# Kernel tuning notes

Hardware: AMD Instinct MI355X
Metric: run time of the kernel (lower is better)

The kernel has to match this reference:

```python
import jax, jax.numpy as jnp
import numpy as np

DIM_K = 32


def setup_inputs() -> dict:
    N, DORI, DAPP, DK, NCLS = 4096, 2048, 512, 32, 21
    key = jax.random.key(0)
    ks = jax.random.split(key, 16)
    std = 0.01
    inp = {
        'rois': jax.random.normal(ks[0], (N, 5), jnp.float32),
        'delta_rois': jax.random.normal(ks[1], (9, N, 5), jnp.float32),
        'features': jax.random.normal(ks[2], (9, N, DORI), jnp.float32),
        'gt_features': jax.random.normal(ks[3], (1, N, DORI), jnp.float32),
        'ious': jax.random.uniform(ks[4], (9, 1, N), jnp.float32),
        # learned parameters (singleton broadcast dims squeezed out)
        'attention_feat': jax.random.normal(ks[5], (DORI, DAPP), jnp.float32) * std,
        'w_k': jax.random.normal(ks[6], (DAPP, DK, 4), jnp.float32) * std,
        'w_q': jax.random.normal(ks[7], (9, DAPP, DK, 4), jnp.float32) * std,
        'alpha_w': jax.random.normal(ks[8], (9, DORI, 4), jnp.float32) * std,
        'bbox_regress': jax.random.normal(ks[9], (9, DORI, 4), jnp.float32) * 0.001,
        'w_k_cls': jax.random.normal(ks[10], (DAPP, DK, 1), jnp.float32) * std,
        'w_q_cls': jax.random.normal(ks[11], (9, DAPP, DK, 1), jnp.float32) * std,
        'alpha_w_cls': jax.random.normal(ks[12], (9, DORI, 1), jnp.float32) * std,
        'cls_score_w': jax.random.normal(ks[13], (9, DORI, NCLS), jnp.float32) * std,
    }
    return inp


def reference(rois, delta_rois, features, gt_features, ious,
              attention_feat, w_k, w_q, alpha_w, bbox_regress,
              w_k_cls, w_q_cls, alpha_w_cls, cls_score_w):
    # features: (9, N, DORI). The torch code materializes (9,N,DORI,DAPP)
    # via broadcast-mul + sum; einsum computes the identical contraction.
    off = jax.nn.relu(jnp.einsum('anf,fd->and', features, attention_feat))  # (9,N,DAPP)

    alpha = jnp.einsum('anf,afc->anc', features, alpha_w)          # (9,N,4)
    offset = jnp.einsum('anf,afc->anc', features, bbox_regress)   # (9,N,4)
    alpha_softmax = jax.nn.softmax(alpha, axis=0)
    delta8 = delta_rois[:, :, 1:5]                                  # (9,N,4)
    delta_pred_offset = delta8 + offset
    output = jnp.sum(delta_pred_offset * alpha_softmax, axis=0)    # (N,4)

    # ---- classification branch ----
    cls_score = jnp.einsum('anf,afc->anc', features, cls_score_w)  # (9,N,NCLS)
    alpha_cls = jnp.einsum('anf,afc->anc', features, alpha_w_cls)  # (9,N,1)
    alpha_softmax_cls = jax.nn.softmax(alpha_cls, axis=0)

    # ---- training-only beta (query/key) attention ----
    query_out = jnp.einsum('and,adkc->ankc', off, w_q)          # (9,N,DK,4)
    query_out_cls = jnp.einsum('and,adkc->ankc', off, w_q_cls)  # (9,N,DK,1)
    gt_off = jax.nn.relu(jnp.einsum('nf,fd->nd', gt_features[0], attention_feat))  # (N,DAPP)
    key_out = jnp.einsum('nd,dkc->nkc', gt_off, w_k)            # (N,DK,4)
    key_out_cls = jnp.einsum('nd,dkc->nkc', gt_off, w_k_cls)    # (N,DK,1)

    scale = 1.0 / np.sqrt(DIM_K).astype(np.float32)
    beta_out = jnp.einsum('ankc,nkc->anc', query_out, key_out) * scale - ious[:, 0, :, None]  # (9,N,4)
    beta_softmax = jax.nn.softmax(beta_out, axis=0)
    beta_out_cls = jnp.einsum('ankc,nkc->anc', query_out_cls, key_out_cls) * scale - ious.reshape(9, -1, 1)  # (9,N,1)
    beta_softmax_cls = jax.nn.softmax(beta_out_cls, axis=0)

    output_beta = jnp.sum(delta_pred_offset * beta_softmax, axis=0)  # (N,4)

    return (output, output_beta, alpha_softmax, beta_softmax,
            delta_pred_offset, delta_pred_offset, alpha, beta_out,
            cls_score, alpha_softmax_cls, beta_softmax_cls, alpha_cls, beta_out_cls)
```

## Files before the change

kernel.cpp:

```cpp
#include <hip/hip_runtime.h>

using u16 = unsigned short;
using s16x8 = __attribute__((ext_vector_type(8))) short;
using f32x4 = __attribute__((ext_vector_type(4))) float;

#define DEVI __device__ __forceinline__

constexpr int AN = 9, NB = 10, NN = 4096, DORI = 2048, DAPP = 512, NCLS = 21, QCOLS = 160;

constexpr size_t O0 = 0;
constexpr size_t O1 = 16384;
constexpr size_t O2 = 32768;
constexpr size_t O3 = 180224;
constexpr size_t O4 = 327680;
constexpr size_t O5 = 475136;
constexpr size_t O6 = 622592;
constexpr size_t O7 = 770048;
constexpr size_t O8 = 917504;
constexpr size_t O9 = 1691648;
constexpr size_t O10 = 1728512;
constexpr size_t O11 = 1765376;
constexpr size_t O12 = 1802240;

constexpr int CAST_B = 36864;
constexpr int ATT_B  = 256;
constexpr int PQ_B   = 3200;
constexpr int PS_B   = 72;
constexpr int GT_B   = 4096;
constexpr int PREP_TOTAL = CAST_B + ATT_B + PQ_B + PS_B + GT_B;

DEVI u16 f2b(float f) {
  unsigned u = __float_as_uint(f);
  unsigned r = (u + 0x7fffu + ((u >> 16) & 1u)) >> 16;
  return (u16)r;
}

DEVI uint4 pack8(float4 u, float4 v) {
  uint4 r;
  r.x = (unsigned)f2b(u.x) | ((unsigned)f2b(u.y) << 16);
  r.y = (unsigned)f2b(u.z) | ((unsigned)f2b(u.w) << 16);
  r.z = (unsigned)f2b(v.x) | ((unsigned)f2b(v.y) << 16);
  r.w = (unsigned)f2b(v.z) | ((unsigned)f2b(v.w) << 16);
  return r;
}

DEVI void gload_lds16(const u16* g, u16* l) {
  __builtin_amdgcn_global_load_lds(
      (const __attribute__((address_space(1))) void*)g,
      (__attribute__((address_space(3))) void*)l, 16, 0, 0);
}

__global__ __launch_bounds__(256) void prep_cast(const float* __restrict__ features,
                                                 const float* __restrict__ att,
                                                 const float* __restrict__ wq,
                                                 const float* __restrict__ wqc,
                                                 const float* __restrict__ wk,
                                                 const float* __restrict__ wkc,
                                                 const float* __restrict__ aw,
                                                 const float* __restrict__ bb,
                                                 const float* __restrict__ awc,
                                                 const float* __restrict__ cw,
                                                 const float* __restrict__ gt,
                                                 u16* __restrict__ featB,
                                                 u16* __restrict__ attB,
                                                 u16* __restrict__ Wq,
                                                 u16* __restrict__ Wsm) {
  __shared__ float tile[64][65];
  const int b = blockIdx.x, tid = threadIdx.x;
  if (b < CAST_B) {
    if (!featB) return;
    long i = (long)b * 256 + tid;
    float4 v0 = ((const float4*)features)[i * 2];
    float4 v1 = ((const float4*)features)[i * 2 + 1];
    ((uint4*)featB)[i] = pack8(v0, v1);
  } else if (b < CAST_B + ATT_B) {
    int b2 = b - CAST_B;
    int d0 = (b2 >> 3) * 64, c0 = (b2 & 7) * 64;
#pragma unroll
    for (int r = 0; r < 16; ++r) {
      int dl = r * 4 + (tid >> 6), cl = tid & 63;
      tile[dl][cl] = att[(size_t)(d0 + dl) * DAPP + c0 + cl];
    }
    __syncthreads();
#pragma unroll
    for (int w = 0; w < 16; ++w) {
      int cl = w * 4 + (tid >> 6), dl = tid & 63;
      attB[(size_t)(c0 + cl) * DORI + d0 + dl] = f2b(tile[dl][cl]);
    }
  } else if (b < CAST_B + ATT_B + PQ_B) {
    int t = (b - CAST_B - ATT_B) * 256 + tid;
    int bq = t / (QCOLS * DAPP);
    int r = t % (QCOLS * DAPP);
    int col = r / DAPP, d = r % DAPP;
    float v;
    if (bq < 9) {
      if (col < 128) v = wq[(size_t)bq * DAPP * 128 + (size_t)d * 128 + col];
      else           v = wqc[(size_t)bq * DAPP * 32 + (size_t)d * 32 + (col - 128)];
    } else {
      if (col < 128) v = wk[(size_t)d * 128 + col];
      else           v = wkc[(size_t)d * 32 + (col - 128)];
    }
    Wq[t] = f2b(v);
  } else if (b < CAST_B + ATT_B + PQ_B + PS_B) {
    int t = (b - CAST_B - ATT_B - PQ_B) * 256 + tid;
    if (t >= AN * DORI) return;
    int a = t / DORI, f = t % DORI;
    u16* Wa = Wsm + (size_t)a * 32 * DORI;
    for (int c = 0; c < 4; ++c)  Wa[c * DORI + f]       = f2b(aw[((size_t)a * DORI + f) * 4 + c]);
    for (int c = 0; c < 4; ++c)  Wa[(4 + c) * DORI + f] = f2b(bb[((size_t)a * DORI + f) * 4 + c]);
    for (int c = 0; c < 21; ++c) Wa[(8 + c) * DORI + f] = f2b(cw[((size_t)a * DORI + f) * 21 + c]);
    Wa[29 * DORI + f] = f2b(awc[(size_t)a * DORI + f]);
    Wa[30 * DORI + f] = 0;
    Wa[31 * DORI + f] = 0;
  } else {
    if (!featB) return;
    long i = (long)(b - CAST_B - ATT_B - PQ_B - PS_B) * 256 + tid;
    float4 v0 = ((const float4*)gt)[i * 2];
    float4 v1 = ((const float4*)gt)[i * 2 + 1];
    ((uint4*)(featB + (size_t)AN * NN * DORI))[i] = pack8(v0, v1);
  }
}

__global__ __launch_bounds__(256) void gemm_main(const u16* __restrict__ featB,
                                                 const u16* __restrict__ attB,
                                                 const u16* __restrict__ Wsm,
                                                 u16* __restrict__ offb,
                                                 float* __restrict__ smallf,
                                                 float* __restrict__ cls_out) {
  __shared__ __align__(16) u16 As[128 * 32];
  __shared__ __align__(16) u16 Bs[128 * 32];

  int bx = blockIdx.x, by = blockIdx.y, bz = blockIdx.z;
  {
    int h = bx + 5 * (by + 32 * bz);
    int l = (h & 7) * 200 + (h >> 3);
    bx = l % 5; l /= 5; by = l % 32; bz = l / 32;
  }
  const int tid = threadIdx.x, lane = tid & 63, w = tid >> 6;
  const bool small = (bx == 4);
  if (small && bz == 9) return;
  const int tileM = by * 128;
  const u16* Ab = featB + ((size_t)bz * NN + tileM) * DORI;
  const u16* Bb = small ? (Wsm + (size_t)bz * 32 * DORI)
                        : (attB + (size_t)bx * 128 * DORI);

  f32x4 accM[4][4], accS[2][2];
#pragma unroll
  for (int i = 0; i < 4; ++i)
#pragma unroll
    for (int j = 0; j < 4; ++j) accM[i][j] = (f32x4){0.f, 0.f, 0.f, 0.f};
#pragma unroll
  for (int i = 0; i < 2; ++i)
#pragma unroll
    for (int j = 0; j < 2; ++j) accS[i][j] = (f32x4){0.f, 0.f, 0.f, 0.f};

  const int wm = w & 1, wn = w >> 1;
  const u16* ArM = As + (wm * 64 + (lane & 15)) * 32 + (lane >> 4) * 8;
  const u16* BrM = Bs + (wn * 64 + (lane & 15)) * 32 + (lane >> 4) * 8;
  const u16* ArS = As + (w * 32 + (lane & 15)) * 32 + (lane >> 4) * 8;
  const u16* BrS = Bs + ((lane & 15)) * 32 + (lane >> 4) * 8;

  for (int k0 = 0; k0 < DORI; k0 += 32) {
#pragma unroll
    for (int i = 0; i < 2; ++i) {
      int c = tid + i * 256;
      gload_lds16(Ab + (size_t)(c >> 2) * DORI + k0 + (c & 3) * 8, As + c * 8);
    }
    if (small) {
      if (tid < 128)
        gload_lds16(Bb + (size_t)(tid >> 2) * DORI + k0 + (tid & 3) * 8, Bs + tid * 8);
    } else {
#pragma unroll
      for (int i = 0; i < 2; ++i) {
        int c = tid + i * 256;
        gload_lds16(Bb + (size_t)(c >> 2) * DORI + k0 + (c & 3) * 8, Bs + c * 8);
      }
    }
    __syncthreads();
    if (small) {
      s16x8 af[2], bf[2];
#pragma unroll
      for (int i = 0; i < 2; ++i) af[i] = *(const s16x8*)(ArS + i * 16 * 32);
#pragma unroll
      for (int j = 0; j < 2; ++j) bf[j] = *(const s16x8*)(BrS + j * 16 * 32);
#pragma unroll
      for (int i = 0; i < 2; ++i)
#pragma unroll
        for (int j = 0; j < 2; ++j)
          accS[i][j] = __builtin_amdgcn_mfma_f32_16x16x32_bf16(af[i], bf[j], accS[i][j], 0, 0, 0);
    } else {
      s16x8 af[4], bf[4];
#pragma unroll
      for (int i = 0; i < 4; ++i) af[i] = *(const s16x8*)(ArM + i * 16 * 32);
#pragma unroll
      for (int j = 0; j < 4; ++j) bf[j] = *(const s16x8*)(BrM + j * 16 * 32);
#pragma unroll
      for (int i = 0; i < 4; ++i)
#pragma unroll
        for (int j = 0; j < 4; ++j)
          accM[i][j] = __builtin_amdgcn_mfma_f32_16x16x32_bf16(af[i], bf[j], accM[i][j], 0, 0, 0);
    }
    __syncthreads();
  }

  if (small) {
#pragma unroll
    for (int i = 0; i < 2; ++i)
#pragma unroll
      for (int j = 0; j < 2; ++j)
#pragma unroll
        for (int q = 0; q < 4; ++q) {
          const int row = tileM + w * 32 + i * 16 + (lane >> 4) * 4 + q;
          const int col = j * 16 + (lane & 15);
          const size_t an = (size_t)bz * NN + row;
          float v = accS[i][j][q];
          smallf[an * 32 + col] = v;
          if (col >= 8 && col <= 28) cls_out[an * 21 + (col - 8)] = v;
        }
  } else {
    const int r0 = tileM + wm * 64 + (lane >> 4) * 4;
    const int c0 = bx * 128 + wn * 64 + (lane & 15);
#pragma unroll
    for (int i = 0; i < 4; ++i)
#pragma unroll
      for (int j = 0; j < 4; ++j)
#pragma unroll
        for (int q = 0; q < 4; ++q)
          offb[((size_t)bz * NN + r0 + i * 16 + q) * DAPP + c0 + j * 16] =
              f2b(fmaxf(accM[i][j][q], 0.f));
  }
}

template<int BM, int BN, int WM, int WN, bool RELU, bool OUTBF, bool SWZ>
__global__ __launch_bounds__(WM * WN * 64)
void gemm_glds(const u16* __restrict__ A, long sA, const u16* __restrict__ B, long sB,
               void* __restrict__ Cv, long sC, int N, int K) {
  constexpr int THREADS = WM * WN * 64;
  constexpr int WTM = BM / WM, WTN = BN / WN;
  constexpr int FM = WTM / 16, FN = WTN / 16;
  constexpr int ACHN = BM * 4, BCHN = BN * 4;
  constexpr int ACH = (ACHN + THREADS - 1) / THREADS;
  constexpr int BCH = (BCHN + THREADS - 1) / THREADS;
  constexpr bool AFULL = (ACHN % THREADS) == 0, BFULL = (BCHN % THREADS) == 0;

  __shared__ __align__(16) u16 As[BM * 32];
  __shared__ __align__(16) u16 Bs[BN * 32];

  int bx = blockIdx.x, by = blockIdx.y, bz = blockIdx.z;
  if constexpr (SWZ) {
    int gx = gridDim.x, gy = gridDim.y;
    int h = bx + gx * (by + gy * bz);
    int nwg = gx * gy * (int)gridDim.z;
    int cpx = nwg >> 3;
    int l = (h & 7) * cpx + (h >> 3);
    bx = l % gx; l /= gx; by = l % gy; bz = l / gy;
  }

  const int tid = threadIdx.x, lane = tid & 63, wave = tid >> 6;
  const int wm = wave % WM, wn = wave / WM;
  const int tileN = bx * BN, tileM = by * BM;
  const u16* Ab = A + (size_t)bz * sA + (size_t)tileM * K;
  const u16* Bb = B + (size_t)bz * sB + (size_t)tileN * K;

  f32x4 acc[FM][FN];
#pragma unroll
  for (int i = 0; i < FM; ++i)
#pragma unroll
    for (int j = 0; j < FN; ++j) acc[i][j] = (f32x4){0.f, 0.f, 0.f, 0.f};

  const u16* Arow = As + (wm * WTM + (lane & 15)) * 32 + (lane >> 4) * 8;
  const u16* Brow = Bs + (wn * WTN + (lane & 15)) * 32 + (lane >> 4) * 8;

  for (int k0 = 0; k0 < K; k0 += 32) {
#pragma unroll
    for (int i = 0; i < ACH; ++i) {
      int c = tid + i * THREADS;
      if (AFULL || c < ACHN)
        gload_lds16(Ab + (size_t)(c >> 2) * K + k0 + (c & 3) * 8, As + c * 8);
    }
#pragma unroll
    for (int i = 0; i < BCH; ++i) {
      int c = tid + i * THREADS;
      if (BFULL || c < BCHN)
        gload_lds16(Bb + (size_t)(c >> 2) * K + k0 + (c & 3) * 8, Bs + c * 8);
    }
    __syncthreads();
    s16x8 af[FM], bfr[FN];
#pragma unroll
    for (int i = 0; i < FM; ++i) af[i] = *(const s16x8*)(Arow + i * 16 * 32);
#pragma unroll
    for (int j = 0; j < FN; ++j) bfr[j] = *(const s16x8*)(Brow + j * 16 * 32);
#pragma unroll
    for (int i = 0; i < FM; ++i)
#pragma unroll
      for (int j = 0; j < FN; ++j)
        acc[i][j] = __builtin_amdgcn_mfma_f32_16x16x32_bf16(af[i], bfr[j], acc[i][j], 0, 0, 0);
    __syncthreads();
  }

  const int r0 = tileM + wm * WTM + (lane >> 4) * 4;
  const int c0 = tileN + wn * WTN + (lane & 15);
#pragma unroll
  for (int i = 0; i < FM; ++i)
#pragma unroll
    for (int j = 0; j < FN; ++j)
#pragma unroll
      for (int q = 0; q < 4; ++q) {
        float v = acc[i][j][q];
        if (RELU) v = fmaxf(v, 0.f);
        size_t idx = (size_t)bz * sC + (size_t)(r0 + i * 16 + q) * N + (c0 + j * 16);
        if (OUTBF) ((u16*)Cv)[idx] = f2b(v);
        else       ((float*)Cv)[idx] = v;
      }
}

template<int BM, int BN, int WM, int WN, bool RELU, bool OUTBF>
__global__ __launch_bounds__(WM * WN * 64)
void gemm_af32(const float* __restrict__ Av, const float* __restrict__ A2v, long sA,
               const u16* __restrict__ B, long sB,
               void* __restrict__ Cv, long sC, int N, int K) {
  constexpr int THREADS = WM * WN * 64;
  constexpr int WTM = BM / WM, WTN = BN / WN;
  constexpr int FM = WTM / 16, FN = WTN / 16;
  constexpr int ACH = (BM * 4) / THREADS;
  constexpr int BCHN = BN * 4;
  constexpr int BCH = (BCHN + THREADS - 1) / THREADS;
  constexpr bool BFULL = (BCHN % THREADS) == 0;

  __shared__ __align__(16) u16 As[BM * 32];
  __shared__ __align__(16) u16 Bs[BN * 32];

  const int tid = threadIdx.x, lane = tid & 63, wave = tid >> 6;
  const int wm = wave % WM, wn = wave / WM;
  const int tileN = blockIdx.x * BN, tileM = blockIdx.y * BM;
  const int batch = blockIdx.z;
  const float* base = (batch < 9) ? (Av + (size_t)batch * sA) : A2v;
  const float* Ab32 = base + (size_t)tileM * K;
  const u16* Bb = B + (size_t)batch * sB + (size_t)tileN * K;

  f32x4 acc[FM][FN];
#pragma unroll
  for (int i = 0; i < FM; ++i)
#pragma unroll
    for (int j = 0; j < FN; ++j) acc[i][j] = (f32x4){0.f, 0.f, 0.f, 0.f};

  uint4 ra[ACH], rb[BCH];
  auto load_t = [&](int k0) {
#pragma unroll
    for (int i = 0; i < ACH; ++i) {
      int c = tid + i * THREADS;
      const float* s = Ab32 + (size_t)(c >> 2) * K + k0 + (c & 3) * 8;
      ra[i] = pack8(*(const float4*)s, *(const float4*)(s + 4));
    }
#pragma unroll
    for (int i = 0; i < BCH; ++i) {
      int c = tid + i * THREADS;
      if (BFULL || c < BCHN)
        rb[i] = *(const uint4*)(Bb + (size_t)(c >> 2) * K + k0 + (c & 3) * 8);
    }
  };

  load_t(0);
  const u16* Arow = As + (wm * WTM + (lane & 15)) * 32 + (lane >> 4) * 8;
  const u16* Brow = Bs + (wn * WTN + (lane & 15)) * 32 + (lane >> 4) * 8;

  for (int k0 = 0; k0 < K; k0 += 32) {
    __syncthreads();
#pragma unroll
    for (int i = 0; i < ACH; ++i)
      *(uint4*)(As + (size_t)(tid + i * THREADS) * 8) = ra[i];
#pragma unroll
    for (int i = 0; i < BCH; ++i) {
      int c = tid + i * THREADS;
      if (BFULL || c < BCHN) *(uint4*)(Bs + (size_t)c * 8) = rb[i];
    }
    __syncthreads();
    if (k0 + 32 < K) load_t(k0 + 32);
    s16x8 af[FM], bfr[FN];
#pragma unroll
    for (int i = 0; i < FM; ++i) af[i] = *(const s16x8*)(Arow + i * 16 * 32);
#pragma unroll
    for (int j = 0; j < FN; ++j) bfr[j] = *(const s16x8*)(Brow + j * 16 * 32);
#pragma unroll
    for (int i = 0; i < FM; ++i)
#pragma unroll
      for (int j = 0; j < FN; ++j)
        acc[i][j] = __builtin_amdgcn_mfma_f32_16x16x32_bf16(af[i], bfr[j], acc[i][j], 0, 0, 0);
  }

  const int r0 = tileM + wm * WTM + (lane >> 4) * 4;
  const int c0 = tileN + wn * WTN + (lane & 15);
#pragma unroll
  for (int i = 0; i < FM; ++i)
#pragma unroll
    for (int j = 0; j < FN; ++j)
#pragma unroll
      for (int q = 0; q < 4; ++q) {
        float v = acc[i][j][q];
        if (RELU) v = fmaxf(v, 0.f);
        size_t idx = (size_t)batch * sC + (size_t)(r0 + i * 16 + q) * N + (c0 + j * 16);
        if (OUTBF) ((u16*)Cv)[idx] = f2b(v);
        else       ((float*)Cv)[idx] = v;
      }
}

__global__ __launch_bounds__(256) void cls_copy(const float* __restrict__ smallf,
                                                float* __restrict__ o) {
  int i = blockIdx.x * blockDim.x + threadIdx.x;
  if (i >= AN * NN * NCLS) return;
  int an = i / NCLS, c = i % NCLS;
  o[i] = smallf[(size_t)an * 32 + 8 + c];
}

__global__ __launch_bounds__(256) void gemm2qb(const u16* __restrict__ offb,
                                               const u16* __restrict__ Wq,
                                               const float* __restrict__ keyf,
                                               const float* __restrict__ ious,
                                               float* __restrict__ betaf,
                                               float* __restrict__ betac) {
  constexpr int BM = 128, BN = 160;
  __shared__ __align__(16) u16 As[BM * 32];
  __shared__ __align__(16) u16 Bs[BN * 32];
  const int tid = threadIdx.x, lane = tid & 63, wave = tid >> 6;
  const int tileM = blockIdx.x * BM;
  const int a = blockIdx.y;
  const u16* Ab = offb + ((size_t)a * NN + tileM) * DAPP;
  const u16* Bb = Wq + (size_t)a * QCOLS * DAPP;

  f32x4 acc[2][10];
#pragma unroll
  for (int i = 0; i < 2; ++i)
#pragma unroll
    for (int j = 0; j < 10; ++j) acc[i][j] = (f32x4){0.f, 0.f, 0.f, 0.f};

  const u16* Arow = As + (wave * 32 + (lane & 15)) * 32 + (lane >> 4) * 8;
  const u16* Brow = Bs + (lane & 15) * 32 + (lane >> 4) * 8;

  for (int k0 = 0; k0 < DAPP; k0 += 32) {
#pragma unroll
    for (int i = 0; i < 2; ++i) {
      int c = tid + i * 256;
      gload_lds16(Ab + (size_t)(c >> 2) * DAPP + k0 + (c & 3) * 8, As + c * 8);
    }
#pragma unroll
    for (int i = 0; i < 3; ++i) {
      int c = tid + i * 256;
      if (c < 640)
        gload_lds16(Bb + (size_t)(c >> 2) * DAPP + k0 + (c & 3) * 8, Bs + c * 8);
    }
    __syncthreads();
    s16x8 af[2], bfr[10];
#pragma unroll
    for (int i = 0; i < 2; ++i) af[i] = *(const s16x8*)(Arow + i * 16 * 32);
#pragma unroll
    for (int j = 0; j < 10; ++j) bfr[j] = *(const s16x8*)(Brow + j * 16 * 32);
#pragma unroll
    for (int i = 0; i < 2; ++i)
#pragma unroll
      for (int j = 0; j < 10; ++j)
        acc[i][j] = __builtin_amdgcn_mfma_f32_16x16x32_bf16(af[i], bfr[j], acc[i][j], 0, 0, 0);
    __syncthreads();
  }

  const float scale = 0.17677669529663687f;
  const int cg = lane & 15;
#pragma unroll
  for (int i = 0; i < 2; ++i)
#pragma unroll
    for (int q = 0; q < 4; ++q) {
      const int row = tileM + wave * 32 + i * 16 + (lane >> 4) * 4 + q;
      const float* kr = keyf + (size_t)row * QCOLS;
      float m = 0.f;
#pragma unroll
      for (int j = 0; j < 8; ++j) m += acc[i][j][q] * kr[cg + j * 16];
      float cl = acc[i][8][q] * kr[128 + cg] + acc[i][9][q] * kr[144 + cg];
      m += __shfl_xor(m, 4); m += __shfl_xor(m, 8);
      cl += __shfl_xor(cl, 1); cl += __shfl_xor(cl, 2);
      cl += __shfl_xor(cl, 4); cl += __shfl_xor(cl, 8);
      const float iou = ious[(size_t)a * NN + row];
      if (cg < 4)  betaf[((size_t)a * NN + row) * 4 + (lane & 3)] = m * scale - iou;
      if (cg == 0) betac[(size_t)a * NN + row] = cl * scale - iou;
    }
}

__global__ __launch_bounds__(256) void finalize(const float* __restrict__ smallf,
                                                const float* __restrict__ beta_ws,
                                                const float* __restrict__ betac_ws,
                                                const float* __restrict__ delta_rois,
                                                float* __restrict__ out) {
  int t = blockIdx.x * 256 + threadIdx.x;
  if (t >= NN * 4) return;
  const int n = t >> 2, c = t & 3;

  {
    float al[9], be[9], dp[9];
    float mA = -1e30f, mB = -1e30f;
    for (int a = 0; a < 9; ++a) {
      size_t an = (size_t)a * NN + n;
      al[a] = smallf[an * 32 + c];
      float off_ = smallf[an * 32 + 4 + c];
      dp[a] = delta_rois[an * 5 + 1 + c] + off_;
      be[a] = beta_ws[an * 4 + c];
      mA = fmaxf(mA, al[a]); mB = fmaxf(mB, be[a]);
    }
    float eA[9], eB[9], sA = 0.f, sB = 0.f;
    for (int a = 0; a < 9; ++a) {
      eA[a] = expf(al[a] - mA); sA += eA[a];
      eB[a] = expf(be[a] - mB); sB += eB[a];
    }
    float rA = 1.f / sA, rB = 1.f / sB;
    float ov = 0.f, obv = 0.f;
    for (int a = 0; a < 9; ++a) {
      size_t an = (size_t)a * NN + n;
      float as_ = eA[a] * rA, bs_ = eB[a] * rB;
      out[O2 + an * 4 + c] = as_;
      out[O3 + an * 4 + c] = bs_;
      out[O4 + an * 4 + c] = dp[a];
      out[O5 + an * 4 + c] = dp[a];
      out[O6 + an * 4 + c] = al[a];
      out[O7 + an * 4 + c] = be[a];
      ov += dp[a] * as_; obv += dp[a] * bs_;
    }
    out[O0 + (size_t)n * 4 + c] = ov;
    out[O1 + (size_t)n * 4 + c] = obv;
  }

  if (c == 0) {
    float ac[9], bc[9];
    float mA = -1e30f, mB = -1e30f;
    for (int a = 0; a < 9; ++a) {
      size_t an = (size_t)a * NN + n;
      ac[a] = smallf[an * 32 + 29];
      bc[a] = betac_ws[an];
      mA = fmaxf(mA, ac[a]); mB = fmaxf(mB, bc[a]);
    }
    float eA[9], eB[9], sA = 0.f, sB = 0.f;
    for (int a = 0; a < 9; ++a) {
      eA[a] = expf(ac[a] - mA); sA += eA[a];
      eB[a] = expf(bc[a] - mB); sB += eB[a];
    }
    float rA = 1.f / sA, rB = 1.f / sB;
    for (int a = 0; a < 9; ++a) {
      size_t an = (size_t)a * NN + n;
      out[O9 + an]  = eA[a] * rA;
      out[O10 + an] = eB[a] * rB;
      out[O11 + an] = ac[a];
      out[O12 + an] = bc[a];
    }
  }
}

extern "C" void kernel_launch(void* const* d_in, const int* in_sizes, int n_in,
                              void* d_out, int out_size, void* d_ws, size_t ws_size,
                              hipStream_t stream) {
  const float* delta_rois = (const float*)d_in[1];
  const float* features   = (const float*)d_in[2];
  const float* gt_features= (const float*)d_in[3];
  const float* ious       = (const float*)d_in[4];
  const float* att        = (const float*)d_in[5];
  const float* w_k        = (const float*)d_in[6];
  const float* w_q        = (const float*)d_in[7];
  const float* alpha_w    = (const float*)d_in[8];
  const float* bbox       = (const float*)d_in[9];
  const float* w_k_cls    = (const float*)d_in[10];
  const float* w_q_cls    = (const float*)d_in[11];
  const float* alpha_w_cls= (const float*)d_in[12];
  const float* cls_w      = (const float*)d_in[13];
  float* out = (float*)d_out;

  char* ws = (char*)d_ws;
  u16* attB    = (u16*)ws;   ws += (size_t)DAPP * DORI * 2;
  u16* Wq      = (u16*)ws;   ws += (size_t)NB * QCOLS * DAPP * 2;
  u16* Wsmall  = (u16*)ws;   ws += (size_t)AN * 32 * DORI * 2;
  u16* offb    = (u16*)ws;   ws += (size_t)NB * NN * DAPP * 2;
  float* smallf= (float*)ws; ws += (size_t)AN * NN * 32 * 4;
  float* keyf  = (float*)ws; ws += (size_t)NN * QCOLS * 4;
  float* betaf = (float*)ws; ws += (size_t)AN * NN * 4 * 4;
  float* betac = (float*)ws; ws += (size_t)AN * NN * 4;
  size_t base_bytes = (size_t)(ws - (char*)d_ws);
  size_t featB_bytes = (size_t)NB * NN * DORI * 2;
  bool big = ws_size >= base_bytes + featB_bytes;
  u16* featB = big ? (u16*)ws : nullptr;

  prep_cast<<<PREP_TOTAL, 256, 0, stream>>>(features, att, w_q, w_q_cls, w_k, w_k_cls,
                                            alpha_w, bbox, alpha_w_cls, cls_w,
                                            gt_features, featB, attB, Wq, Wsmall);

  if (big) {
    dim3 gm(5, 32, NB);
    gemm_main<<<gm, 256, 0, stream>>>(featB, attB, Wsmall, offb, smallf, out + O8);
  } else {
    dim3 g1(DAPP / 128, NN / 128, NB);
    gemm_af32<128, 128, 2, 2, true, true><<<g1, 256, 0, stream>>>(
        features, gt_features, (long)NN * DORI, attB, 0, offb, (long)NN * DAPP, DAPP, DORI);
    dim3 gsm(1, NN / 128, AN);
    gemm_af32<128, 32, 4, 1, false, false><<<gsm, 256, 0, stream>>>(
        features, nullptr, (long)NN * DORI, Wsmall, (long)32 * DORI,
        smallf, (long)NN * 32, 32, DORI);
    cls_copy<<<(AN * NN * NCLS + 255) / 256, 256, 0, stream>>>(smallf, out + O8);
  }

  dim3 gk(QCOLS / 32, NN / 128, 1);
  gemm_glds<128, 32, 4, 1, false, false, false><<<gk, 256, 0, stream>>>(
      offb + (size_t)9 * NN * DAPP, 0, Wq + (size_t)9 * QCOLS * DAPP, 0,
      keyf, 0, QCOLS, DAPP);

  dim3 g2(NN / 128, AN, 1);
  gemm2qb<<<g2, 256, 0, stream>>>(offb, Wq, keyf, ious, betaf, betac);

  finalize<<<NN * 4 / 256, 256, 0, stream>>>(smallf, betaf, betac, delta_rois, out);
}
```

Baseline: 334.2 us.

## Double-buffer LDS tiles in GEMM kernels to overlap global loads with MFMA

Applies the same change to gemm_main, gemm_glds and gemm2qb. Each gets two shared-memory buffers for its A and B tiles. The next K-slice is loaded with the asynchronous global-to-LDS copy into the other buffer while MFMAs run on the current one, and the barrier before compute is removed, leaving one __syncthreads per iteration. The aim is to hide global load latency behind the matrix math. In exchange, LDS use per block doubles, which may lower occupancy. The compiler may also insert conservative waits before LDS reads, which would cancel the overlap.

```diff
diff --git a/kernel.cpp b/kernel.cpp
--- a/kernel.cpp
+++ b/kernel.cpp
@@ -127,8 +127,8 @@
                                                  u16* __restrict__ offb,
                                                  float* __restrict__ smallf,
                                                  float* __restrict__ cls_out) {
-  __shared__ __align__(16) u16 As[128 * 32];
-  __shared__ __align__(16) u16 Bs[128 * 32];
+  __shared__ __align__(16) u16 As[2][128 * 32];
+  __shared__ __align__(16) u16 Bs[2][128 * 32];
 
   int bx = blockIdx.x, by = blockIdx.y, bz = blockIdx.z;
   {
@@ -155,29 +155,35 @@
     for (int j = 0; j < 2; ++j) accS[i][j] = (f32x4){0.f, 0.f, 0.f, 0.f};
 
   const int wm = w & 1, wn = w >> 1;
-  const u16* ArM = As + (wm * 64 + (lane & 15)) * 32 + (lane >> 4) * 8;
-  const u16* BrM = Bs + (wn * 64 + (lane & 15)) * 32 + (lane >> 4) * 8;
-  const u16* ArS = As + (w * 32 + (lane & 15)) * 32 + (lane >> 4) * 8;
-  const u16* BrS = Bs + ((lane & 15)) * 32 + (lane >> 4) * 8;
-
-  for (int k0 = 0; k0 < DORI; k0 += 32) {
+
+  auto stage = [&](int buf, int k0) {
 #pragma unroll
     for (int i = 0; i < 2; ++i) {
       int c = tid + i * 256;
-      gload_lds16(Ab + (size_t)(c >> 2) * DORI + k0 + (c & 3) * 8, As + c * 8);
+      gload_lds16(Ab + (size_t)(c >> 2) * DORI + k0 + (c & 3) * 8, As[buf] + c * 8);
     }
     if (small) {
       if (tid < 128)
-        gload_lds16(Bb + (size_t)(tid >> 2) * DORI + k0 + (tid & 3) * 8, Bs + tid * 8);
+        gload_lds16(Bb + (size_t)(tid >> 2) * DORI + k0 + (tid & 3) * 8, Bs[buf] + tid * 8);
     } else {
 #pragma unroll
       for (int i = 0; i < 2; ++i) {
         int c = tid + i * 256;
-        gload_lds16(Bb + (size_t)(c >> 2) * DORI + k0 + (c & 3) * 8, Bs + c * 8);
+        gload_lds16(Bb + (size_t)(c >> 2) * DORI + k0 + (c & 3) * 8, Bs[buf] + c * 8);
       }
     }
-    __syncthreads();
+  };
+
+  stage(0, 0);
+  __syncthreads();
+  int cur = 0;
+  for (int k0 = 0; k0 < DORI; k0 += 32) {
+    if (k0 + 32 < DORI) stage(cur ^ 1, k0 + 32);
+    const u16* Asb = As[cur];
+    const u16* Bsb = Bs[cur];
     if (small) {
+      const u16* ArS = Asb + (w * 32 + (lane & 15)) * 32 + (lane >> 4) * 8;
+      const u16* BrS = Bsb + ((lane & 15)) * 32 + (lane >> 4) * 8;
       s16x8 af[2], bf[2];
 #pragma unroll
       for (int i = 0; i < 2; ++i) af[i] = *(const s16x8*)(ArS + i * 16 * 32);
@@ -189,6 +195,8 @@
         for (int j = 0; j < 2; ++j)
           accS[i][j] = __builtin_amdgcn_mfma_f32_16x16x32_bf16(af[i], bf[j], accS[i][j], 0, 0, 0);
     } else {
+      const u16* ArM = Asb + (wm * 64 + (lane & 15)) * 32 + (lane >> 4) * 8;
+      const u16* BrM = Bsb + (wn * 64 + (lane & 15)) * 32 + (lane >> 4) * 8;
       s16x8 af[4], bf[4];
 #pragma unroll
       for (int i = 0; i < 4; ++i) af[i] = *(const s16x8*)(ArM + i * 16 * 32);
@@ -201,6 +209,7 @@
           accM[i][j] = __builtin_amdgcn_mfma_f32_16x16x32_bf16(af[i], bf[j], accM[i][j], 0, 0, 0);
     }
     __syncthreads();
+    cur ^= 1;
   }
 
   if (small) {
@@ -243,8 +252,8 @@
   constexpr int BCH = (BCHN + THREADS - 1) / THREADS;
   constexpr bool AFULL = (ACHN % THREADS) == 0, BFULL = (BCHN % THREADS) == 0;
 
-  __shared__ __align__(16) u16 As[BM * 32];
-  __shared__ __align__(16) u16 Bs[BN * 32];
+  __shared__ __align__(16) u16 As[2][BM * 32];
+  __shared__ __align__(16) u16 Bs[2][BN * 32];
 
   int bx = blockIdx.x, by = blockIdx.y, bz = blockIdx.z;
   if constexpr (SWZ) {
@@ -268,23 +277,28 @@
 #pragma unroll
     for (int j = 0; j < FN; ++j) acc[i][j] = (f32x4){0.f, 0.f, 0.f, 0.f};
 
-  const u16* Arow = As + (wm * WTM + (lane & 15)) * 32 + (lane >> 4) * 8;
-  const u16* Brow = Bs + (wn * WTN + (lane & 15)) * 32 + (lane >> 4) * 8;
-
-  for (int k0 = 0; k0 < K; k0 += 32) {
+  auto stage = [&](int buf, int k0) {
 #pragma unroll
     for (int i = 0; i < ACH; ++i) {
       int c = tid + i * THREADS;
       if (AFULL || c < ACHN)
-        gload_lds16(Ab + (size_t)(c >> 2) * K + k0 + (c & 3) * 8, As + c * 8);
+        gload_lds16(Ab + (size_t)(c >> 2) * K + k0 + (c & 3) * 8, As[buf] + c * 8);
     }
 #pragma unroll
     for (int i = 0; i < BCH; ++i) {
       int c = tid + i * THREADS;
       if (BFULL || c < BCHN)
-        gload_lds16(Bb + (size_t)(c >> 2) * K + k0 + (c & 3) * 8, Bs + c * 8);
-    }
-    __syncthreads();
+        gload_lds16(Bb + (size_t)(c >> 2) * K + k0 + (c & 3) * 8, Bs[buf] + c * 8);
+    }
+  };
+
+  stage(0, 0);
+  __syncthreads();
+  int cur = 0;
+  for (int k0 = 0; k0 < K; k0 += 32) {
+    if (k0 + 32 < K) stage(cur ^ 1, k0 + 32);
+    const u16* Arow = As[cur] + (wm * WTM + (lane & 15)) * 32 + (lane >> 4) * 8;
+    const u16* Brow = Bs[cur] + (wn * WTN + (lane & 15)) * 32 + (lane >> 4) * 8;
     s16x8 af[FM], bfr[FN];
 #pragma unroll
     for (int i = 0; i < FM; ++i) af[i] = *(const s16x8*)(Arow + i * 16 * 32);
@@ -296,6 +310,7 @@
       for (int j = 0; j < FN; ++j)
         acc[i][j] = __builtin_amdgcn_mfma_f32_16x16x32_bf16(af[i], bfr[j], acc[i][j], 0, 0, 0);
     __syncthreads();
+    cur ^= 1;
   }
 
   const int r0 = tileM + wm * WTM + (lane >> 4) * 4;
@@ -419,8 +434,8 @@
                                                float* __restrict__ betaf,
                                                float* __restrict__ betac) {
   constexpr int BM = 128, BN = 160;
-  __shared__ __align__(16) u16 As[BM * 32];
-  __shared__ __align__(16) u16 Bs[BN * 32];
+  __shared__ __align__(16) u16 As[2][BM * 32];
+  __shared__ __align__(16) u16 Bs[2][BN * 32];
   const int tid = threadIdx.x, lane = tid & 63, wave = tid >> 6;
   const int tileM = blockIdx.x * BM;
   const int a = blockIdx.y;
@@ -433,22 +448,27 @@
 #pragma unroll
     for (int j = 0; j < 10; ++j) acc[i][j] = (f32x4){0.f, 0.f, 0.f, 0.f};
 
-  const u16* Arow = As + (wave * 32 + (lane & 15)) * 32 + (lane >> 4) * 8;
-  const u16* Brow = Bs + (lane & 15) * 32 + (lane >> 4) * 8;
-
-  for (int k0 = 0; k0 < DAPP; k0 += 32) {
+  auto stage = [&](int buf, int k0) {
 #pragma unroll
     for (int i = 0; i < 2; ++i) {
       int c = tid + i * 256;
-      gload_lds16(Ab + (size_t)(c >> 2) * DAPP + k0 + (c & 3) * 8, As + c * 8);
+      gload_lds16(Ab + (size_t)(c >> 2) * DAPP + k0 + (c & 3) * 8, As[buf] + c * 8);
     }
 #pragma unroll
     for (int i = 0; i < 3; ++i) {
       int c = tid + i * 256;
       if (c < 640)
-        gload_lds16(Bb + (size_t)(c >> 2) * DAPP + k0 + (c & 3) * 8, Bs + c * 8);
-    }
-    __syncthreads();
+        gload_lds16(Bb + (size_t)(c >> 2) * DAPP + k0 + (c & 3) * 8, Bs[buf] + c * 8);
+    }
+  };
+
+  stage(0, 0);
+  __syncthreads();
+  int cur = 0;
+  for (int k0 = 0; k0 < DAPP; k0 += 32) {
+    if (k0 + 32 < DAPP) stage(cur ^ 1, k0 + 32);
+    const u16* Arow = As[cur] + (wave * 32 + (lane & 15)) * 32 + (lane >> 4) * 8;
+    const u16* Brow = Bs[cur] + (lane & 15) * 32 + (lane >> 4) * 8;
     s16x8 af[2], bfr[10];
 #pragma unroll
     for (int i = 0; i < 2; ++i) af[i] = *(const s16x8*)(Arow + i * 16 * 32);
@@ -460,6 +480,7 @@
       for (int j = 0; j < 10; ++j)
         acc[i][j] = __builtin_amdgcn_mfma_f32_16x16x32_bf16(af[i], bfr[j], acc[i][j], 0, 0, 0);
     __syncthreads();
+    cur ^= 1;
   }
 
   const float scale = 0.17677669529663687f;
```

Result: slower. 349.0 us (+4.4%).
